# Optimization experiments

Hardware: AMD Instinct MI355X
Metric: run time of the kernel (lower is better)

The kernel has to match this reference:

```python
import math
import jax, jax.numpy as jnp
import numpy as np

DIM = 1024
HEADS = 16
HEAD_DIM = DIM // HEADS
NEG = -10000.0


def setup_inputs() -> dict:
    key = jax.random.key(0)
    ks = jax.random.split(key, 9)
    B, S = 2, 2048
    s = 1.0 / math.sqrt(DIM)
    inp = {
        "x": jax.random.normal(ks[0], (B, S, DIM), dtype=jnp.float32),
        "Wq": jax.random.normal(ks[1], (DIM, DIM), dtype=jnp.float32) * s,
        "bq": jnp.zeros((DIM,), dtype=jnp.float32),
        "Wk": jax.random.normal(ks[2], (DIM, DIM), dtype=jnp.float32) * s,
        "bk": jnp.zeros((DIM,), dtype=jnp.float32),
        "Wv": jax.random.normal(ks[3], (DIM, DIM), dtype=jnp.float32) * s,
        "bv": jnp.zeros((DIM,), dtype=jnp.float32),
        "Wo": jax.random.normal(ks[4], (DIM, DIM), dtype=jnp.float32) * s,
        "bo": jnp.zeros((DIM,), dtype=jnp.float32),
    }
    return inp


def reference(x, Wq, bq, Wk, bk, Wv, bv, Wo, bo):
    B, S, D = x.shape
    q = x @ Wq + bq
    k = x @ Wk + bk
    v = x @ Wv + bv
    # [B, H, S, hd]
    def split_heads(t):
        return t.reshape(B, S, HEADS, HEAD_DIM).transpose(0, 2, 1, 3)
    q, k, v = split_heads(q), split_heads(k), split_heads(v)
    scores = jnp.einsum("bhqd,bhkd->bhqk", q, k) / math.sqrt(HEAD_DIM)
    causal = jnp.tril(jnp.ones((S, S), dtype=bool))  # [S, S]
    scores = jnp.where(causal[None, None], scores, NEG)
    probs = jax.nn.softmax(scores, axis=-1)
    ctx = jnp.einsum("bhqk,bhkd->bhqd", probs, v)  # [B, H, S, hd]
    ctx = ctx.transpose(0, 2, 1, 3).reshape(B, S, D)
    out = ctx @ Wo + bo
    return out
```

## Files before the change

kernel.cpp:

```cpp
#include <hip/hip_runtime.h>
#include <hip/hip_bf16.h>
#include <math.h>

#define DIMX 1024
#define HEADSX 16
#define HDX 64
#define BBX 2
#define SSX 2048
#define MMX (BBX*SSX)

typedef __bf16 bf16x8 __attribute__((ext_vector_type(8)));
typedef __bf16 bf16x4 __attribute__((ext_vector_type(4)));
typedef float  f32x4  __attribute__((ext_vector_type(4)));

#define NEGF (-1e30f)
#define QSCALE 0.18033688011112042f

static __device__ __forceinline__ void gload16(const void* g, void* l) {
  __builtin_amdgcn_global_load_lds(
      (const __attribute__((address_space(1))) unsigned int*)g,
      (__attribute__((address_space(3))) unsigned int*)l, 16, 0, 0);
}

__global__ __launch_bounds__(256) void k_prep(
    const float* __restrict__ x, const float* __restrict__ Wq,
    const float* __restrict__ Wk, const float* __restrict__ Wv,
    const float* __restrict__ Wo, __bf16* __restrict__ xb,
    __bf16* __restrict__ wqkvT, __bf16* __restrict__ woT) {
  const int bid = blockIdx.x;
  if (bid < 2048) {
    int i = (bid * 256 + threadIdx.x) * 8;
    float4 v0 = *(const float4*)&x[i];
    float4 v1 = *(const float4*)&x[i + 4];
    bf16x8 o = { (__bf16)v0.x, (__bf16)v0.y, (__bf16)v0.z, (__bf16)v0.w,
                 (__bf16)v1.x, (__bf16)v1.y, (__bf16)v1.z, (__bf16)v1.w };
    *(bf16x8*)&xb[i] = o;
    return;
  }
  __shared__ __bf16 tile[64][65];
  const int wb = bid - 2048;
  const int mat = wb >> 8, t8 = wb & 255;
  const float* src = (mat == 0) ? Wq : (mat == 1) ? Wk : (mat == 2) ? Wv : Wo;
  __bf16* dst = (mat < 3) ? (wqkvT + (size_t)mat * DIMX * DIMX) : woT;
  const int tx = t8 & 15, ty = t8 >> 4;
  const int k0 = ty * 64, n0 = tx * 64;
  #pragma unroll
  for (int rep = 0; rep < 16; ++rep) {
    int idx = rep * 256 + threadIdx.x;
    int r = idx >> 6, c = idx & 63;
    tile[r][c] = (__bf16)src[(size_t)(k0 + r) * DIMX + n0 + c];
  }
  __syncthreads();
  #pragma unroll
  for (int rep = 0; rep < 16; ++rep) {
    int idx = rep * 256 + threadIdx.x;
    int r = idx >> 6, c = idx & 63;
    dst[(size_t)(n0 + r) * DIMX + k0 + c] = tile[c][r];
  }
}

__global__ __launch_bounds__(256) void k_gemm_qkv(
    const __bf16* __restrict__ A,
    const __bf16* __restrict__ Bt,
    const float* __restrict__ b0, const float* __restrict__ b1,
    const float* __restrict__ b2,
    __bf16* __restrict__ qb, __bf16* __restrict__ kb, __bf16* __restrict__ vtb) {
  constexpr int BK = 32, K = 1024;
  __shared__ __bf16 As[2][128 * BK];
  __shared__ __bf16 Bs[2][128 * BK];
  const int tid = threadIdx.x, lane = tid & 63, wave = tid >> 6;
  const int g = lane >> 4, r16 = lane & 15;
  const int wm = wave & 1, wn = wave >> 1;
  const int id = blockIdx.x;
  const int xcd = id & 7, j96 = id >> 3;
  const int m0 = (xcd * 4 + (j96 & 3)) * 128;
  const int n0 = (j96 >> 2) * 128;

  auto STAGE = [&](int buf, int k0) {
    #pragma unroll
    for (int i = 0; i < 2; ++i) {
      int c = wave * 64 + lane + 256 * i;
      gload16(&A [(size_t)(m0 + (c >> 2)) * K + k0 + (c & 3) * 8],
              (char*)As[buf] + (size_t)(wave * 64 + 256 * i) * 16);
      gload16(&Bt[(size_t)(n0 + (c >> 2)) * K + k0 + (c & 3) * 8],
              (char*)Bs[buf] + (size_t)(wave * 64 + 256 * i) * 16);
    }
  };

  f32x4 acc[4][4] = {};

  STAGE(0, 0);
  int cur = 0;
  for (int k0 = 0; k0 < K; k0 += BK, cur ^= 1) {
    __syncthreads();
    if (k0 + BK < K) STAGE(cur ^ 1, k0 + BK);
    bf16x8 af[4], bfr[4];
    #pragma unroll
    for (int i = 0; i < 4; ++i)
      af[i]  = *(const bf16x8*)&As[cur][(wm * 64 + i * 16 + r16) * BK + g * 8];
    #pragma unroll
    for (int j = 0; j < 4; ++j)
      bfr[j] = *(const bf16x8*)&Bs[cur][(wn * 64 + j * 16 + r16) * BK + g * 8];
    #pragma unroll
    for (int i = 0; i < 4; ++i)
      #pragma unroll
      for (int j = 0; j < 4; ++j)
        acc[i][j] = __builtin_amdgcn_mfma_f32_16x16x32_bf16(af[i], bfr[j],
                                                            acc[i][j], 0, 0, 0);
  }

  #pragma unroll
  for (int i = 0; i < 4; ++i) {
    #pragma unroll
    for (int j = 0; j < 4; ++j) {
      #pragma unroll
      for (int r = 0; r < 4; ++r) {
        int m = m0 + wm * 64 + i * 16 + 4 * g + r;
        int n = n0 + wn * 64 + j * 16 + r16;
        float v = acc[i][j][r];
        int proj = n >> 10, w = n & 1023, h = w >> 6, d = w & 63;
        const float* bp = (proj == 0) ? b0 : (proj == 1) ? b1 : b2;
        v += bp[w];
        int b = m >> 11, s = m & 2047, bh = b * HEADSX + h;
        if (proj == 0)      qb [((size_t)bh * SSX + s) * HDX + d] =
                                (__bf16)(v * QSCALE);
        else if (proj == 1) kb [((size_t)bh * SSX + s) * HDX + d] = (__bf16)v;
        else                vtb[((size_t)bh * HDX + d) * SSX + s] = (__bf16)v;
      }
    }
  }
}

__global__ __launch_bounds__(256) void k_gemm_out(
    const __bf16* __restrict__ A,
    const __bf16* __restrict__ Bt,
    const float* __restrict__ bias, float* __restrict__ outf) {
  constexpr int BK = 32, K = 1024;
  __shared__ __bf16 As[2][128 * BK];
  __shared__ __bf16 Bs[2][64 * BK];
  const int tid = threadIdx.x, lane = tid & 63, wave = tid >> 6;
  const int g = lane >> 4, r16 = lane & 15;
  const int wm = wave & 1, wn = wave >> 1;
  const int id = blockIdx.x;
  const int xcd = id & 7, j64 = id >> 3;
  const int m0 = (xcd * 4 + (j64 & 3)) * 128;
  const int n0 = (j64 >> 2) * 64;

  auto STAGE = [&](int buf, int k0) {
    #pragma unroll
    for (int i = 0; i < 2; ++i) {
      int c = wave * 64 + lane + 256 * i;
      gload16(&A [(size_t)(m0 + (c >> 2)) * K + k0 + (c & 3) * 8],
              (char*)As[buf] + (size_t)(wave * 64 + 256 * i) * 16);
    }
    {
      int c = tid;
      gload16(&Bt[(size_t)(n0 + (c >> 2)) * K + k0 + (c & 3) * 8],
              (char*)Bs[buf] + (size_t)(wave * 64) * 16);
    }
  };

  f32x4 acc[4][2] = {};

  STAGE(0, 0);
  int cur = 0;
  for (int k0 = 0; k0 < K; k0 += BK, cur ^= 1) {
    __syncthreads();
    if (k0 + BK < K) STAGE(cur ^ 1, k0 + BK);
    bf16x8 af[4], bfr[2];
    #pragma unroll
    for (int i = 0; i < 4; ++i)
      af[i]  = *(const bf16x8*)&As[cur][(wm * 64 + i * 16 + r16) * BK + g * 8];
    #pragma unroll
    for (int j = 0; j < 2; ++j)
      bfr[j] = *(const bf16x8*)&Bs[cur][(wn * 32 + j * 16 + r16) * BK + g * 8];
    #pragma unroll
    for (int i = 0; i < 4; ++i)
      #pragma unroll
      for (int j = 0; j < 2; ++j)
        acc[i][j] = __builtin_amdgcn_mfma_f32_16x16x32_bf16(af[i], bfr[j],
                                                            acc[i][j], 0, 0, 0);
  }

  #pragma unroll
  for (int i = 0; i < 4; ++i)
    #pragma unroll
    for (int j = 0; j < 2; ++j)
      #pragma unroll
      for (int r = 0; r < 4; ++r) {
        int m = m0 + wm * 64 + i * 16 + 4 * g + r;
        int n = n0 + wn * 32 + j * 16 + r16;
        outf[(size_t)m * DIMX + n] = acc[i][j][r] + bias[n];
      }
}

__global__ __launch_bounds__(256, 2) void k_attn(
    const __bf16* __restrict__ qb, const __bf16* __restrict__ kb,
    const __bf16* __restrict__ vtb, __bf16* __restrict__ ctxb) {
  const int tid = threadIdx.x;
  const int lane = tid & 63, wq = tid >> 6;
  const int g = lane >> 4, r16 = lane & 15;

  const int id = blockIdx.x;
  const int xcd = id & 7, idx = id >> 3;
  const int bh = xcd * 4 + (idx & 3);
  const int p  = idx >> 2;
  const int b = bh >> 4, h = bh & 15;

  const int ntL = p + 1, ntH = 32 - p;
  const int q0L = p * 64 + wq * 16;
  const int q0H = (31 - p) * 64 + wq * 16;

  const __bf16* Q  = qb  + (size_t)bh * SSX * HDX;
  const __bf16* Kp = kb  + (size_t)bh * SSX * HDX;
  const __bf16* Vt = vtb + (size_t)bh * HDX * SSX;

  __shared__ __bf16 Ks[2][64 * 64];
  __shared__ __bf16 Vs[2][64 * 64];
  __shared__ unsigned Pld[4][512];

  bf16x8 qfL[2], qfH[2];
  qfL[0] = *(const bf16x8*)&Q[(size_t)(q0L + r16) * HDX + g * 8];
  qfL[1] = *(const bf16x8*)&Q[(size_t)(q0L + r16) * HDX + 32 + g * 8];
  qfH[0] = *(const bf16x8*)&Q[(size_t)(q0H + r16) * HDX + g * 8];
  qfH[1] = *(const bf16x8*)&Q[(size_t)(q0H + r16) * HDX + 32 + g * 8];

  f32x4 accL[4] = {}, accH[4] = {};
  float mrunL = NEGF, lrunL = 0.f;
  float mrunH = NEGF, lrunH = 0.f;

  auto STAGE = [&](int buf, int t) {
    const int kv0 = t * 64;
    #pragma unroll
    for (int i = 0; i < 2; ++i) {
      int c = tid + 256 * i;
      int r = c >> 3;
      int cb = (c & 7) ^ (r & 7);
      gload16(&Kp[(size_t)(kv0 + r) * HDX + cb * 8],
              (char*)Ks[buf] + (size_t)(wq * 64 + 256 * i) * 16);
      gload16(&Vt[(size_t)r * SSX + kv0 + cb * 8],
              (char*)Vs[buf] + (size_t)(wq * 64 + 256 * i) * 16);
    }
  };

  auto SUBTILE = [&](const bf16x8* qf, f32x4* acc, float& mrun, float& lrun,
                     int qrow, bool last, int kv0, int cur) {
    f32x4 sac[4] = {};
    __builtin_amdgcn_s_setprio(1);
    #pragma unroll
    for (int kk = 0; kk < 2; ++kk)
      #pragma unroll
      for (int jj = 0; jj < 4; ++jj) {
        int rr = jj * 16 + r16;
        bf16x8 kf = *(const bf16x8*)
            &Ks[cur][rr * 64 + (((kk << 2) + g) ^ (rr & 7)) * 8];
        sac[jj] = __builtin_amdgcn_mfma_f32_16x16x32_bf16(kf, qf[kk], sac[jj],
                                                          0, 0, 0);
      }
    __builtin_amdgcn_s_setprio(0);

    float pv[4][4];
    float mt = NEGF;
    #pragma unroll
    for (int jj = 0; jj < 4; ++jj)
      #pragma unroll
      for (int r = 0; r < 4; ++r) {
        float s = sac[jj][r];
        if (last) {
          int kcol = kv0 + jj * 16 + 4 * g + r;
          s = (kcol > qrow) ? NEGF : s;
        }
        pv[jj][r] = s;
        mt = fmaxf(mt, s);
      }
    mt = fmaxf(mt, __shfl_xor(mt, 16));
    mt = fmaxf(mt, __shfl_xor(mt, 32));

    if (__any(mt > mrun)) {
      float mnew = fmaxf(mrun, mt);
      float fac = exp2f(mrun - mnew);
      mrun = mnew;
      lrun *= fac;
      #pragma unroll
      for (int j2 = 0; j2 < 4; ++j2)
        #pragma unroll
        for (int r = 0; r < 4; ++r)
          acc[j2][r] *= fac;
    }
    float rs = 0.f;
    #pragma unroll
    for (int jj = 0; jj < 4; ++jj)
      #pragma unroll
      for (int r = 0; r < 4; ++r) {
        float px = exp2f(pv[jj][r] - mrun);
        pv[jj][r] = px;
        rs += px;
      }
    lrun += rs;

    #pragma unroll
    for (int jj = 0; jj < 4; ++jj)
      #pragma unroll
      for (int rp = 0; rp < 2; ++rp) {
        unsigned w;
        asm("v_cvt_pk_bf16_f32 %0, %1, %2"
            : "=v"(w) : "v"(pv[jj][2 * rp]), "v"(pv[jj][2 * rp + 1]));
        int c = jj * 8 + g * 2 + rp;
        int addr = r16 * 32 + (((c >> 2) ^ (r16 & 7)) << 2) + (c & 3);
        Pld[wq][addr] = w;
      }

    bf16x8 pf[2];
    #pragma unroll
    for (int half = 0; half < 2; ++half) {
      int c = half * 16 + g * 4;
      int addr = r16 * 32 + (((c >> 2) ^ (r16 & 7)) << 2);
      pf[half] = *(const bf16x8*)&Pld[wq][addr];
    }
    __builtin_amdgcn_s_setprio(1);
    #pragma unroll
    for (int j2 = 0; j2 < 4; ++j2)
      #pragma unroll
      for (int half = 0; half < 2; ++half) {
        int dd = j2 * 16 + r16;
        bf16x8 vf = *(const bf16x8*)
            &Vs[cur][dd * 64 + (((half << 2) + g) ^ (dd & 7)) * 8];
        acc[j2] = __builtin_amdgcn_mfma_f32_16x16x32_bf16(vf, pf[half],
                                                          acc[j2], 0, 0, 0);
      }
    __builtin_amdgcn_s_setprio(0);
  };

  STAGE(0, 0);
  __syncthreads();

  for (int t = 0; t < ntH; ++t) {
    const int cur = t & 1;
    if (t + 1 < ntH) STAGE(cur ^ 1, t + 1);
    const int kv0 = t * 64;

    SUBTILE(qfH, accH, mrunH, lrunH, q0H + r16, t == ntH - 1, kv0, cur);
    if (t < ntL)
      SUBTILE(qfL, accL, mrunL, lrunL, q0L + r16, t == ntL - 1, kv0, cur);

    __syncthreads();
  }

  auto EPIL = [&](f32x4* acc, float lrun, int q0) {
    lrun += __shfl_xor(lrun, 16);
    lrun += __shfl_xor(lrun, 32);
    const float inv = 1.f / lrun;
    const int s = q0 + r16;
    #pragma unroll
    for (int j2 = 0; j2 < 4; ++j2)
      #pragma unroll
      for (int r = 0; r < 4; ++r) {
        int d = j2 * 16 + 4 * g + r;
        ctxb[((size_t)(b * SSX + s)) * DIMX + h * HDX + d] =
            (__bf16)(acc[j2][r] * inv);
      }
  };
  EPIL(accH, lrunH, q0H);
  EPIL(accL, lrunL, q0L);
}

extern "C" void kernel_launch(void* const* d_in, const int* in_sizes, int n_in,
                              void* d_out, int out_size, void* d_ws,
                              size_t ws_size, hipStream_t stream) {
  const float* x  = (const float*)d_in[0];
  const float* Wq = (const float*)d_in[1];
  const float* bq = (const float*)d_in[2];
  const float* Wk = (const float*)d_in[3];
  const float* bk = (const float*)d_in[4];
  const float* Wv = (const float*)d_in[5];
  const float* bv = (const float*)d_in[6];
  const float* Wo = (const float*)d_in[7];
  const float* bo = (const float*)d_in[8];
  float* out = (float*)d_out;

  char* ws = (char*)d_ws;
  __bf16* xb    = (__bf16*)(ws);
  __bf16* wqkvT = (__bf16*)(ws + ((size_t)8  << 20));
  __bf16* woT   = (__bf16*)(ws + ((size_t)14 << 20));
  __bf16* qb    = (__bf16*)(ws + ((size_t)16 << 20));
  __bf16* kb    = (__bf16*)(ws + ((size_t)24 << 20));
  __bf16* vtb   = (__bf16*)(ws + ((size_t)32 << 20));
  __bf16* ctxb  = xb;

  k_prep<<<3072, 256, 0, stream>>>(x, Wq, Wk, Wv, Wo, xb, wqkvT, woT);
  k_gemm_qkv<<<768, 256, 0, stream>>>(xb, wqkvT, bq, bk, bv, qb, kb, vtb);
  k_attn<<<512, 256, 0, stream>>>(qb, kb, vtb, ctxb);
  k_gemm_out<<<512, 256, 0, stream>>>(ctxb, woT, bo, out);
}
```

Measured before the change: 121.9 us.

## Split attention KV loop across two blocks with merge; single-buffer GEMM staging

Attention blocks now split the KV tile loop into even and odd halves when the workspace is large enough, doubling the grid to 1024 blocks. Each half writes normalized bf16 partials plus max/sum to the workspace, and a new merge kernel combines them. Separately, both GEMM kernels drop LDS double buffering for a simpler load-sync-compute loop, which removes overlap of loads with MFMA but halves shared memory. This trades extra global traffic and a launch for more parallelism, and adds bf16 rounding of the partials.

New measurement: 130.2 us (median of 2 runs). +6.8%, slower.

```diff
diff --git a/kernel.cpp b/kernel.cpp
--- a/kernel.cpp
+++ b/kernel.cpp
@@ -66,8 +66,8 @@
     const float* __restrict__ b2,
     __bf16* __restrict__ qb, __bf16* __restrict__ kb, __bf16* __restrict__ vtb) {
   constexpr int BK = 32, K = 1024;
-  __shared__ __bf16 As[2][128 * BK];
-  __shared__ __bf16 Bs[2][128 * BK];
+  __shared__ __bf16 As[128 * BK];
+  __shared__ __bf16 Bs[128 * BK];
   const int tid = threadIdx.x, lane = tid & 63, wave = tid >> 6;
   const int g = lane >> 4, r16 = lane & 15;
   const int wm = wave & 1, wn = wave >> 1;
@@ -76,31 +76,26 @@
   const int m0 = (xcd * 4 + (j96 & 3)) * 128;
   const int n0 = (j96 >> 2) * 128;
 
-  auto STAGE = [&](int buf, int k0) {
+  f32x4 acc[4][4] = {};
+
+  for (int k0 = 0; k0 < K; k0 += BK) {
+    __syncthreads();
     #pragma unroll
     for (int i = 0; i < 2; ++i) {
       int c = wave * 64 + lane + 256 * i;
       gload16(&A [(size_t)(m0 + (c >> 2)) * K + k0 + (c & 3) * 8],
-              (char*)As[buf] + (size_t)(wave * 64 + 256 * i) * 16);
+              (char*)As + (size_t)(wave * 64 + 256 * i) * 16);
       gload16(&Bt[(size_t)(n0 + (c >> 2)) * K + k0 + (c & 3) * 8],
-              (char*)Bs[buf] + (size_t)(wave * 64 + 256 * i) * 16);
-    }
-  };
-
-  f32x4 acc[4][4] = {};
-
-  STAGE(0, 0);
-  int cur = 0;
-  for (int k0 = 0; k0 < K; k0 += BK, cur ^= 1) {
+              (char*)Bs + (size_t)(wave * 64 + 256 * i) * 16);
+    }
     __syncthreads();
-    if (k0 + BK < K) STAGE(cur ^ 1, k0 + BK);
     bf16x8 af[4], bfr[4];
     #pragma unroll
     for (int i = 0; i < 4; ++i)
-      af[i]  = *(const bf16x8*)&As[cur][(wm * 64 + i * 16 + r16) * BK + g * 8];
+      af[i]  = *(const bf16x8*)&As[(wm * 64 + i * 16 + r16) * BK + g * 8];
     #pragma unroll
     for (int j = 0; j < 4; ++j)
-      bfr[j] = *(const bf16x8*)&Bs[cur][(wn * 64 + j * 16 + r16) * BK + g * 8];
+      bfr[j] = *(const bf16x8*)&Bs[(wn * 64 + j * 16 + r16) * BK + g * 8];
     #pragma unroll
     for (int i = 0; i < 4; ++i)
       #pragma unroll
@@ -136,8 +131,8 @@
     const __bf16* __restrict__ Bt,
     const float* __restrict__ bias, float* __restrict__ outf) {
   constexpr int BK = 32, K = 1024;
-  __shared__ __bf16 As[2][128 * BK];
-  __shared__ __bf16 Bs[2][64 * BK];
+  __shared__ __bf16 As[128 * BK];
+  __shared__ __bf16 Bs[64 * BK];
   const int tid = threadIdx.x, lane = tid & 63, wave = tid >> 6;
   const int g = lane >> 4, r16 = lane & 15;
   const int wm = wave & 1, wn = wave >> 1;
@@ -146,34 +141,29 @@
   const int m0 = (xcd * 4 + (j64 & 3)) * 128;
   const int n0 = (j64 >> 2) * 64;
 
-  auto STAGE = [&](int buf, int k0) {
+  f32x4 acc[4][2] = {};
+
+  for (int k0 = 0; k0 < K; k0 += BK) {
+    __syncthreads();
     #pragma unroll
     for (int i = 0; i < 2; ++i) {
       int c = wave * 64 + lane + 256 * i;
       gload16(&A [(size_t)(m0 + (c >> 2)) * K + k0 + (c & 3) * 8],
-              (char*)As[buf] + (size_t)(wave * 64 + 256 * i) * 16);
+              (char*)As + (size_t)(wave * 64 + 256 * i) * 16);
     }
     {
       int c = tid;
       gload16(&Bt[(size_t)(n0 + (c >> 2)) * K + k0 + (c & 3) * 8],
-              (char*)Bs[buf] + (size_t)(wave * 64) * 16);
-    }
-  };
-
-  f32x4 acc[4][2] = {};
-
-  STAGE(0, 0);
-  int cur = 0;
-  for (int k0 = 0; k0 < K; k0 += BK, cur ^= 1) {
+              (char*)Bs + (size_t)(wave * 64) * 16);
+    }
     __syncthreads();
-    if (k0 + BK < K) STAGE(cur ^ 1, k0 + BK);
     bf16x8 af[4], bfr[2];
     #pragma unroll
     for (int i = 0; i < 4; ++i)
-      af[i]  = *(const bf16x8*)&As[cur][(wm * 64 + i * 16 + r16) * BK + g * 8];
+      af[i]  = *(const bf16x8*)&As[(wm * 64 + i * 16 + r16) * BK + g * 8];
     #pragma unroll
     for (int j = 0; j < 2; ++j)
-      bfr[j] = *(const bf16x8*)&Bs[cur][(wn * 32 + j * 16 + r16) * BK + g * 8];
+      bfr[j] = *(const bf16x8*)&Bs[(wn * 32 + j * 16 + r16) * BK + g * 8];
     #pragma unroll
     for (int i = 0; i < 4; ++i)
       #pragma unroll
@@ -194,17 +184,24 @@
       }
 }
 
+template<int SPLIT>
 __global__ __launch_bounds__(256, 2) void k_attn(
     const __bf16* __restrict__ qb, const __bf16* __restrict__ kb,
-    const __bf16* __restrict__ vtb, __bf16* __restrict__ ctxb) {
+    const __bf16* __restrict__ vtb, __bf16* __restrict__ ctxb,
+    __bf16* __restrict__ pacc, float* __restrict__ pml) {
   const int tid = threadIdx.x;
   const int lane = tid & 63, wq = tid >> 6;
   const int g = lane >> 4, r16 = lane & 15;
 
   const int id = blockIdx.x;
-  const int xcd = id & 7, idx = id >> 3;
-  const int bh = xcd * 4 + (idx & 3);
-  const int p  = idx >> 2;
+  const int xcd = id & 7;
+  int rest = id >> 3;
+  const int bh = xcd * 4 + (rest & 3);
+  rest >>= 2;
+  int p, s;
+  if constexpr (SPLIT) { p = rest >> 1; s = rest & 1; }
+  else                 { p = rest;      s = 0;        }
+  constexpr int TSTEP = SPLIT ? 2 : 1;
   const int b = bh >> 4, h = bh & 15;
 
   const int ntL = p + 1, ntH = 32 - p;
@@ -265,13 +262,13 @@
     for (int jj = 0; jj < 4; ++jj)
       #pragma unroll
       for (int r = 0; r < 4; ++r) {
-        float s = sac[jj][r];
+        float sv = sac[jj][r];
         if (last) {
           int kcol = kv0 + jj * 16 + 4 * g + r;
-          s = (kcol > qrow) ? NEGF : s;
+          sv = (kcol > qrow) ? NEGF : sv;
         }
-        pv[jj][r] = s;
-        mt = fmaxf(mt, s);
+        pv[jj][r] = sv;
+        mt = fmaxf(mt, sv);
       }
     mt = fmaxf(mt, __shfl_xor(mt, 16));
     mt = fmaxf(mt, __shfl_xor(mt, 32));
@@ -331,12 +328,13 @@
     __builtin_amdgcn_s_setprio(0);
   };
 
-  STAGE(0, 0);
+  STAGE(0, s);
   __syncthreads();
 
-  for (int t = 0; t < ntH; ++t) {
-    const int cur = t & 1;
-    if (t + 1 < ntH) STAGE(cur ^ 1, t + 1);
+  int it = 0;
+  for (int t = s; t < ntH; t += TSTEP, ++it) {
+    const int cur = it & 1;
+    if (t + TSTEP < ntH) STAGE(cur ^ 1, t + TSTEP);
     const int kv0 = t * 64;
 
     SUBTILE(qfH, accH, mrunH, lrunH, q0H + r16, t == ntH - 1, kv0, cur);
@@ -346,22 +344,61 @@
     __syncthreads();
   }
 
-  auto EPIL = [&](f32x4* acc, float lrun, int q0) {
+  auto EPIL = [&](f32x4* acc, float mrun, float lrun, int q0) {
     lrun += __shfl_xor(lrun, 16);
     lrun += __shfl_xor(lrun, 32);
-    const float inv = 1.f / lrun;
-    const int s = q0 + r16;
-    #pragma unroll
-    for (int j2 = 0; j2 < 4; ++j2)
-      #pragma unroll
-      for (int r = 0; r < 4; ++r) {
-        int d = j2 * 16 + 4 * g + r;
-        ctxb[((size_t)(b * SSX + s)) * DIMX + h * HDX + d] =
-            (__bf16)(acc[j2][r] * inv);
-      }
+    const float inv = (lrun > 0.f) ? 1.f / lrun : 0.f;
+    const int q = q0 + r16;
+    if constexpr (SPLIT) {
+      size_t base = ((size_t)(s * 32 + bh) * SSX + q) * HDX;
+      #pragma unroll
+      for (int j2 = 0; j2 < 4; ++j2)
+        #pragma unroll
+        for (int r = 0; r < 4; ++r)
+          pacc[base + j2 * 16 + 4 * g + r] = (__bf16)(acc[j2][r] * inv);
+      if (lane < 16) {
+        size_t mb = ((size_t)(s * 32 + bh) * SSX + q) * 2;
+        pml[mb] = mrun;
+        pml[mb + 1] = lrun;
+      }
+    } else {
+      #pragma unroll
+      for (int j2 = 0; j2 < 4; ++j2)
+        #pragma unroll
+        for (int r = 0; r < 4; ++r) {
+          int d = j2 * 16 + 4 * g + r;
+          ctxb[((size_t)(b * SSX + q)) * DIMX + h * HDX + d] =
+              (__bf16)(acc[j2][r] * inv);
+        }
+    }
   };
-  EPIL(accH, lrunH, q0H);
-  EPIL(accL, lrunL, q0L);
+  EPIL(accH, mrunH, lrunH, q0H);
+  EPIL(accL, mrunL, lrunL, q0L);
+}
+
+__global__ __launch_bounds__(256) void k_merge(
+    const __bf16* __restrict__ pacc, const float* __restrict__ pml,
+    __bf16* __restrict__ ctxb) {
+  int idx = blockIdx.x * 256 + threadIdx.x;
+  int d8 = idx & 7, rest = idx >> 3;
+  int q = rest & 2047, bh = rest >> 11;
+  size_t r0 = (size_t)bh * SSX + q;
+  size_t r1 = (size_t)(32 + bh) * SSX + q;
+  bf16x8 a0 = *(const bf16x8*)&pacc[r0 * HDX + d8 * 8];
+  bf16x8 a1 = *(const bf16x8*)&pacc[r1 * HDX + d8 * 8];
+  float m0 = pml[r0 * 2], l0 = pml[r0 * 2 + 1];
+  float m1 = pml[r1 * 2], l1 = pml[r1 * 2 + 1];
+  float M = fmaxf(m0, m1);
+  float w0 = l0 * exp2f(m0 - M);
+  float w1 = l1 * exp2f(m1 - M);
+  float inv = 1.f / (w0 + w1);
+  w0 *= inv; w1 *= inv;
+  bf16x8 o;
+  #pragma unroll
+  for (int i = 0; i < 8; ++i)
+    o[i] = (__bf16)((float)a0[i] * w0 + (float)a1[i] * w1);
+  int b = bh >> 4, h = bh & 15;
+  *(bf16x8*)&ctxb[((size_t)(b * SSX + q)) * DIMX + h * HDX + d8 * 8] = o;
 }
 
 extern "C" void kernel_launch(void* const* d_in, const int* in_sizes, int n_in,
@@ -385,10 +422,19 @@
   __bf16* qb    = (__bf16*)(ws + ((size_t)16 << 20));
   __bf16* kb    = (__bf16*)(ws + ((size_t)24 << 20));
   __bf16* vtb   = (__bf16*)(ws + ((size_t)32 << 20));
+  __bf16* pacc  = (__bf16*)(ws + ((size_t)40 << 20));
+  float*  pml   = (float*) (ws + ((size_t)56 << 20));
   __bf16* ctxb  = xb;
+
+  const bool splitk = ws_size >= ((size_t)57 << 20);
 
   k_prep<<<3072, 256, 0, stream>>>(x, Wq, Wk, Wv, Wo, xb, wqkvT, woT);
   k_gemm_qkv<<<768, 256, 0, stream>>>(xb, wqkvT, bq, bk, bv, qb, kb, vtb);
-  k_attn<<<512, 256, 0, stream>>>(qb, kb, vtb, ctxb);
+  if (splitk) {
+    k_attn<1><<<1024, 256, 0, stream>>>(qb, kb, vtb, nullptr, pacc, pml);
+    k_merge<<<2048, 256, 0, stream>>>(pacc, pml, ctxb);
+  } else {
+    k_attn<0><<<512, 256, 0, stream>>>(qb, kb, vtb, ctxb, nullptr, nullptr);
+  }
   k_gemm_out<<<512, 256, 0, stream>>>(ctxb, woT, bo, out);
 }
```
